# Kernel optimization log

Hardware: AMD Instinct MI355X
Metric: run time of the kernel (lower is better)

## Reference

```python
import jax, jax.numpy as jnp
import numpy as np

NQ = 16               # num_qubits
S = 1 << NQ           # 65536 superposition states
D = 128               # quantum_dim
B = 4                 # batch
ENT = 0.8             # entanglement_strength
DECO_T = 100.0        # decoherence_time


def setup_inputs() -> dict:
    key = jax.random.key(0)
    ks = jax.random.split(key, 7)
    return {
        "input_features": jax.random.normal(ks[0], (B, D), jnp.float32),
        # complex quantum_weights, stored as separate real/imag parts
        "qw_re": jax.random.normal(ks[1], (S, D), jnp.float32),
        "qw_im": jax.random.normal(ks[2], (S, D), jnp.float32),
        "rotation_angles": jax.random.normal(ks[3], (NQ, 3), jnp.float32),
        "entanglement_matrix": jax.random.normal(ks[4], (NQ, NQ), jnp.float32),
        # per-qubit measurement Linear(D, D): y = x @ W_i.T + b_i
        "meas_W": jax.random.normal(ks[5], (NQ, D, D), jnp.float32) / np.sqrt(D).astype(np.float32),
        "meas_b": jax.random.normal(ks[6], (NQ, D), jnp.float32) * np.float32(0.01),
    }


def reference(input_features, qw_re, qw_im, rotation_angles, entanglement_matrix, meas_W, meas_b):
    b = input_features.shape[0]  # input is only consulted for batch size (as in the original)
    qw = qw_re + 1j * qw_im                              # [S, D] complex64
    # ---- apply_quantum_gates: cumulative per-qubit phase = exp(i * sum of all angles)
    phase = jnp.exp(1j * rotation_angles.sum())
    state = jnp.broadcast_to((qw * phase)[None], (b, S, D))  # [B, S, D]
    # entanglement: softmax(16x16) mixes across a qubit-factored view of the state dim
    ew = jax.nn.softmax(entanglement_matrix, axis=-1).astype(state.dtype)  # [NQ, NQ]
    ent = jnp.einsum('qp,bpkd->bqkd', ew, state.reshape(b, NQ, S // NQ, D)).reshape(b, S, D)
    state = ENT * ent + (1.0 - ENT) * state
    # ---- simulate_decoherence (timer = 1 on first call)
    coh = jnp.exp(jnp.float32(-1.0 / DECO_T))
    kn = jax.random.split(jax.random.key(1), 3)
    inv_sqrt2 = np.float32(1.0 / np.sqrt(2.0))
    noise = (jax.random.normal(kn[0], (b, S, D)) + 1j * jax.random.normal(kn[1], (b, S, D))) \
            * (inv_sqrt2 * (1.0 - coh) * np.float32(0.1))
    state = state * coh + noise
    # ---- quantum_measurement: one categorical draw over S states per (batch, column)
    # multinomial(p[:, j], 1) == Gumbel-max over log p; normalization constant cancels.
    logits = jnp.log(jnp.real(state) ** 2 + jnp.imag(state) ** 2 + 1e-20)  # log |amp|^2, [B,S,D]
    u = jax.random.uniform(kn[2], (b, S, D), minval=1e-7, maxval=1.0)
    idx = jnp.argmax(logits - jnp.log(-jnp.log(u)), axis=1)  # [B, D] sampled state index
    # one-hot collapsed state; only rows 0..NQ-1 are consumed by the measurement ops,
    # so we avoid materializing the full [B, S, D] one-hot.
    measured = (idx[:, None, :] == jnp.arange(NQ)[None, :, None]).astype(jnp.float32)  # [B, NQ, D]
    outs = jnp.einsum('bnd,ned->bne', measured, meas_W) + meas_b[None]  # per-qubit Linear
    return outs.mean(axis=1)  # [B, D]
```

## Files before the change

kernel.cpp:

```cpp
#include <hip/hip_runtime.h>
#include <stdint.h>
#include <math.h>

constexpr int D_ = 128;
constexpr int KDIM = 4096;
constexpr uint32_t NTH = 4096u * 128u;

#define DELTA   0.00385f
#define RELM    1.0002f
#define WLO_PAD 1e-3f
#define EPS_CMP 1e-3f

__host__ __device__ static inline void tfround(uint32_t& x0, uint32_t& x1, int r) {
    x0 += x1;
    x1 = (x1 << r) | (x1 >> (32 - r));
    x1 ^= x0;
}

__host__ __device__ static inline void tf2x32(uint32_t k0, uint32_t k1,
                                              uint32_t x0, uint32_t x1,
                                              uint32_t& o0, uint32_t& o1) {
    uint32_t ks2 = k0 ^ k1 ^ 0x1BD11BDAu;
    x0 += k0; x1 += k1;
    tfround(x0, x1, 13); tfround(x0, x1, 15); tfround(x0, x1, 26); tfround(x0, x1, 6);
    x0 += k1;  x1 += ks2 + 1u;
    tfround(x0, x1, 17); tfround(x0, x1, 29); tfround(x0, x1, 16); tfround(x0, x1, 24);
    x0 += ks2; x1 += k0 + 2u;
    tfround(x0, x1, 13); tfround(x0, x1, 15); tfround(x0, x1, 26); tfround(x0, x1, 6);
    x0 += k0;  x1 += k1 + 3u;
    tfround(x0, x1, 17); tfround(x0, x1, 29); tfround(x0, x1, 16); tfround(x0, x1, 24);
    x0 += k1;  x1 += ks2 + 4u;
    tfround(x0, x1, 13); tfround(x0, x1, 15); tfround(x0, x1, 26); tfround(x0, x1, 6);
    x0 += ks2; x1 += k0 + 5u;
    o0 = x0; o1 = x1;
}

__device__ __forceinline__ float neglog_hybrid(float u, float nz) {
    float p4 = fmaf(nz, 0.2f, 0.25f);
    float p3 = fmaf(nz, p4, 0.33333334f);
    float p2 = fmaf(nz, p3, 0.5f);
    float poly = fmaf(nz, p2, 1.0f);
    float ts = nz * poly;
    float tl = -__logf(u);
    return (nz < 0.01f) ? ts : tl;
}

__device__ __forceinline__ float erfinv_fast(float x) {
    float w = -__logf(fmaf(-x, x, 1.0f));
    float p;
    if (w < 5.0f) {
        w -= 2.5f;
        p = 2.81022636e-08f;
        p = fmaf(p, w, 3.43273939e-07f);
        p = fmaf(p, w, -3.5233877e-06f);
        p = fmaf(p, w, -4.39150654e-06f);
        p = fmaf(p, w, 0.00021858087f);
        p = fmaf(p, w, -0.00125372503f);
        p = fmaf(p, w, -0.00417768164f);
        p = fmaf(p, w, 0.246640727f);
        p = fmaf(p, w, 1.50140941f);
    } else {
        float wt = -__logf((1.0f - x) * (1.0f + x));
        float v = sqrtf(wt) - 3.0f;
        p = -0.000200214257f;
        p = fmaf(p, v, 0.000100950558f);
        p = fmaf(p, v, 0.00134934322f);
        p = fmaf(p, v, -0.00367342844f);
        p = fmaf(p, v, 0.00573950773f);
        p = fmaf(p, v, -0.0076224613f);
        p = fmaf(p, v, 0.00943887047f);
        p = fmaf(p, v, 1.00167406f);
        p = fmaf(p, v, 2.83297682f);
    }
    return p * x;
}

__device__ __forceinline__ uint32_t ordmap(float x) {
    uint32_t u = __float_as_uint(x);
    return (u & 0x80000000u) ? ~u : (u | 0x80000000u);
}
__device__ __forceinline__ float ordunmap(uint32_t m) {
    uint32_t u = (m & 0x80000000u) ? (m & 0x7FFFFFFFu) : ~m;
    return __uint_as_float(u);
}

__global__ __launch_bounds__(512) void qsl_prep(const float* __restrict__ ang,
                                                const float* __restrict__ ent,
                                                float* __restrict__ ws_f,
                                                unsigned long long* __restrict__ keys,
                                                uint32_t* __restrict__ Mlo,
                                                float coh) {
    __shared__ float sm[16][16];
    int t = threadIdx.x;
    keys[t] = 0ULL;
    if (t < 512) Mlo[t] = 0u;
    if (t < 16) {
        float row[16];
        float m = -INFINITY;
        for (int j = 0; j < 16; j++) { row[j] = ent[t * 16 + j]; m = fmaxf(m, row[j]); }
        float s = 0.f;
        for (int j = 0; j < 16; j++) { row[j] = expf(row[j] - m); s += row[j]; }
        float inv = 1.0f / s;
        for (int j = 0; j < 16; j++) sm[t][j] = row[j] * inv;
    }
    if (t == 0) {
        float a = 0.f;
        for (int i = 0; i < 48; i++) a += ang[i];
        ws_f[256] = cosf(a);
        ws_f[257] = sinf(a);
    }
    __syncthreads();
    if (t < 256) {
        int q = t >> 4, p = t & 15;
        float c = (0.8f * coh) * sm[q][p];
        if (q == p) c += 0.2f * coh;
        ws_f[t] = c;
    }
}

__global__ __launch_bounds__(256) void qsl_bound(const float* __restrict__ qre,
                                                 const float* __restrict__ qim,
                                                 const float* __restrict__ Cg,
                                                 uint32_t* __restrict__ Mlo,
                                                 unsigned long long* __restrict__ maskArr,
                                                 float4* __restrict__ whiArr,
                                                 uint32_t kC0, uint32_t kC1) {
    const int d = threadIdx.x;
    const int y = threadIdx.y;
    const int kk = blockIdx.x * 2 + y;
    const uint32_t g = (uint32_t)kk * 128u + (uint32_t)d;

    const float pr = Cg[256], pi = Cg[257];

    float eLo[16], eHi[16];
    {
        float vr[16], vi[16];
#pragma unroll
        for (int p = 0; p < 16; p++) {
            int off = (p * KDIM + kk) * D_ + d;
            float ar = qre[off], ai = qim[off];
            vr[p] = fmaf(pr, ar, -(pi * ai));
            vi[p] = fmaf(pi, ar, pr * ai);
        }
#pragma unroll
        for (int q = 0; q < 16; q++) {
            float br = 0.f, bi = 0.f;
#pragma unroll
            for (int p = 0; p < 16; p++) {
                float c = Cg[q * 16 + p];
                br = fmaf(c, vr[p], br);
                bi = fmaf(c, vi[p], bi);
            }
            float abr = fabsf(br), abi = fabsf(bi);
            float hr = abr + DELTA, hq = abi + DELTA;
            float Phi_hi = fmaf(hr, hr, fmaf(hq, hq, 1e-20f));
            float lr = fmaxf(abr - DELTA, 0.f), lq = fmaxf(abi - DELTA, 0.f);
            float Phi_lo = fmaf(lr, lr, fmaf(lq, lq, 1e-20f));
            eLo[q] = __builtin_amdgcn_rcpf(Phi_lo);
            eHi[q] = __builtin_amdgcn_rcpf(Phi_hi);
        }
    }

    unsigned long long mask64 = 0ull;
    float whi_a[4];

#pragma unroll 1
    for (int b = 0; b < 4; b++) {
        const uint32_t nb = g + ((uint32_t)b << 23);
        float ph[16];
        float mlo_t = INFINITY, mhi_t = INFINITY;
#pragma unroll
        for (int q = 0; q < 16; q++) {
            uint32_t w0, w1;
            tf2x32(kC0, kC1, 0u, nb + ((uint32_t)q << 19), w0, w1);
            uint32_t r = w0 ^ w1;
            float f = __uint_as_float((r >> 9) | 0x3f800000u) - 1.0f;
            float nz = 1.0f - f;
            float t = neglog_hybrid(f, nz);
            float plo = t * eLo[q];
            float phi_ = t * eHi[q];
            ph[q] = phi_;
            mlo_t = fminf(mlo_t, plo);
            mhi_t = fminf(mhi_t, phi_);
        }
        uint32_t mloc = 0u;
        float thr = mlo_t * RELM;
#pragma unroll
        for (int q = 0; q < 16; q++)
            if (ph[q] <= thr) mloc |= (1u << q);
        mask64 |= ((unsigned long long)mloc) << (b * 16);

        float wlo = -__logf(mlo_t) - WLO_PAD;
        whi_a[b]  = -__logf(mhi_t);
        uint32_t mu = ordmap(wlo);
        uint32_t cur = Mlo[b * 128 + d];
        if (mu > cur) atomicMax(&Mlo[b * 128 + d], mu);
    }

    maskArr[g] = mask64;
    whiArr[g] = make_float4(whi_a[0], whi_a[1], whi_a[2], whi_a[3]);
}

__global__ __launch_bounds__(256) void qsl_resolve(const float* __restrict__ qre,
                                                   const float* __restrict__ qim,
                                                   const float* __restrict__ Cg,
                                                   const uint32_t* __restrict__ Mlo,
                                                   const unsigned long long* __restrict__ maskArr,
                                                   const float4* __restrict__ whiArr,
                                                   unsigned long long* __restrict__ keys,
                                                   uint32_t kA0, uint32_t kA1,
                                                   uint32_t kB0, uint32_t kB1,
                                                   uint32_t kC0, uint32_t kC1,
                                                   float nc) {
    const int d = threadIdx.x;
    const int y = threadIdx.y;
    const int kk = blockIdx.x * 2 + y;
    const uint32_t g = (uint32_t)kk * 128u + (uint32_t)d;

    unsigned long long mask64 = maskArr[g];
    float4 whi4 = whiArr[g];
    uint32_t m0 = Mlo[0 * 128 + d];
    uint32_t m1 = Mlo[1 * 128 + d];
    uint32_t m2 = Mlo[2 * 128 + d];
    uint32_t m3 = Mlo[3 * 128 + d];

    unsigned long long live = 0ull;
    if (!(whi4.x < ordunmap(m0) - EPS_CMP)) live |= 0xFFFFull;
    if (!(whi4.y < ordunmap(m1) - EPS_CMP)) live |= 0xFFFFull << 16;
    if (!(whi4.z < ordunmap(m2) - EPS_CMP)) live |= 0xFFFFull << 32;
    if (!(whi4.w < ordunmap(m3) - EPS_CMP)) live |= 0xFFFFull << 48;
    mask64 &= live;
    if (mask64 == 0ull) return;

    const float pr = Cg[256], pi = Cg[257];
    float vr[16], vi[16];
#pragma unroll
    for (int p = 0; p < 16; p++) {
        int off = (p * KDIM + kk) * D_ + d;
        float ar = qre[off], ai = qim[off];
        vr[p] = fmaf(pr, ar, -(pi * ai));
        vi[p] = fmaf(pi, ar, pr * ai);
    }

    const float ULO = 1e-7f;
    const float UDF = 1.0f - 1e-7f;
    const float NLO = -0.99999994f;
    const float NDF = 1.0f - NLO;

    while (mask64) {
        int bit = __ffsll(mask64) - 1;
        mask64 &= mask64 - 1ull;
        uint32_t q = (uint32_t)bit & 15u;
        int b = bit >> 4;
        uint32_t n = g + ((uint32_t)bit << 19);

        float br = 0.f, bi = 0.f;
        const float4* C4 = reinterpret_cast<const float4*>(Cg + (q << 4));
#pragma unroll
        for (int j = 0; j < 4; j++) {
            float4 c = C4[j];
            br = fmaf(c.x, vr[j*4+0], br); bi = fmaf(c.x, vi[j*4+0], bi);
            br = fmaf(c.y, vr[j*4+1], br); bi = fmaf(c.y, vi[j*4+1], bi);
            br = fmaf(c.z, vr[j*4+2], br); bi = fmaf(c.z, vi[j*4+2], bi);
            br = fmaf(c.w, vr[j*4+3], br); bi = fmaf(c.w, vi[j*4+3], bi);
        }

        uint32_t w0, w1;
        tf2x32(kC0, kC1, 0u, n, w0, w1);
        uint32_t rC = w0 ^ w1;
        tf2x32(kA0, kA1, 0u, n, w0, w1);
        uint32_t rA = w0 ^ w1;
        tf2x32(kB0, kB1, 0u, n, w0, w1);
        uint32_t rB = w0 ^ w1;

        float fu = __uint_as_float((rC >> 9) | 0x3f800000u) - 1.0f;
        float u  = __fadd_rn(__fmul_rn(fu, UDF), ULO);
        float f0 = __uint_as_float((rA >> 9) | 0x3f800000u) - 1.0f;
        float x0 = __fadd_rn(__fmul_rn(f0, NDF), NLO);
        float f1 = __uint_as_float((rB >> 9) | 0x3f800000u) - 1.0f;
        float x1 = __fadd_rn(__fmul_rn(f1, NDF), NLO);
        float nr = 1.41421356f * erfinv_fast(x0);
        float ni = 1.41421356f * erfinv_fast(x1);
        float ar = fmaf(nc, nr, br);
        float ai = fmaf(nc, ni, bi);
        float logit = __logf(fmaf(ar, ar, fmaf(ai, ai, 1e-20f)));
        float nz = 1.0f - u;
        float t = neglog_hybrid(u, nz);
        float gv = __logf(t);
        float v = logit - gv;

        uint32_t s = (q << 12) + (uint32_t)kk;
        uint32_t mu = ordmap(v);
        unsigned long long kp =
            ((unsigned long long)mu << 32) |
            (unsigned long long)(0xFFFFFFFFu - s);
        atomicMax(&keys[b * 128 + d], kp);
    }
}

__global__ __launch_bounds__(128) void qsl_out(const unsigned long long* __restrict__ keys,
                                               const float* __restrict__ mW,
                                               const float* __restrict__ mb,
                                               float* __restrict__ out) {
    int b = blockIdx.x, e = threadIdx.x;
    __shared__ uint32_t idx_s[128];
    unsigned long long kp = keys[b * 128 + e];
    idx_s[e] = 0xFFFFFFFFu - (uint32_t)(kp & 0xFFFFFFFFull);
    __syncthreads();

    float acc = 0.f;
#pragma unroll
    for (int n = 0; n < 16; n++) acc += mb[n * 128 + e];
    for (int dd = 0; dd < 128; dd++) {
        uint32_t m = idx_s[dd];
        if (m < 16u) acc += mW[(m * 128 + e) * 128 + dd];
    }
    out[b * 128 + e] = acc * 0.0625f;
}

extern "C" void kernel_launch(void* const* d_in, const int* in_sizes, int n_in,
                              void* d_out, int out_size, void* d_ws, size_t ws_size,
                              hipStream_t stream) {
    (void)in_sizes; (void)n_in; (void)out_size; (void)ws_size;
    const float* qre = (const float*)d_in[1];
    const float* qim = (const float*)d_in[2];
    const float* ang = (const float*)d_in[3];
    const float* ent = (const float*)d_in[4];
    const float* mW  = (const float*)d_in[5];
    const float* mb  = (const float*)d_in[6];
    float* out = (float*)d_out;

    char* ws = (char*)d_ws;
    float* ws_f = (float*)ws;
    unsigned long long* keys = (unsigned long long*)(ws + 4096);
    uint32_t* Mlo = (uint32_t*)(ws + 8192);
    unsigned long long* maskArr = (unsigned long long*)(ws + 12288);
    float4* whiArr = (float4*)(ws + 12288 + (size_t)NTH * 8);

    uint32_t kn[6];
    tf2x32(0u, 1u, 0u, 0u, kn[0], kn[1]);
    tf2x32(0u, 1u, 0u, 1u, kn[2], kn[3]);
    tf2x32(0u, 1u, 0u, 2u, kn[4], kn[5]);

    float coh = expf(-0.01f);
    float nc  = (0.70710678f * (1.0f - coh)) * 0.1f;

    hipLaunchKernelGGL(qsl_prep, dim3(1), dim3(512), 0, stream, ang, ent, ws_f, keys, Mlo, coh);
    hipLaunchKernelGGL(qsl_bound, dim3(2048), dim3(128, 2), 0, stream,
                       qre, qim, ws_f, Mlo, maskArr, whiArr, kn[4], kn[5]);
    hipLaunchKernelGGL(qsl_resolve, dim3(2048), dim3(128, 2), 0, stream,
                       qre, qim, ws_f, Mlo, maskArr, whiArr, keys,
                       kn[0], kn[1], kn[2], kn[3], kn[4], kn[5], nc);
    hipLaunchKernelGGL(qsl_out, dim3(4), dim3(128), 0, stream, keys, mW, mb, out);
}
```

Measured before the change: 114.8 us.

## Restructure bound kernel to loop over qubits with 4-way batched Threefry and LDS-parked bounds

```diff
diff --git a/kernel.cpp b/kernel.cpp
--- a/kernel.cpp
+++ b/kernel.cpp
@@ -7,7 +7,7 @@
 constexpr uint32_t NTH = 4096u * 128u;
 
 #define DELTA   0.00385f
-#define RELM    1.0002f
+#define RELB    1.0101f
 #define WLO_PAD 1e-3f
 #define EPS_CMP 1e-3f
 
@@ -33,6 +33,41 @@
     tfround(x0, x1, 13); tfround(x0, x1, 15); tfround(x0, x1, 26); tfround(x0, x1, 6);
     x0 += ks2; x1 += k0 + 5u;
     o0 = x0; o1 = x1;
+}
+
+__device__ __forceinline__ void tf4round(uint32_t x0[4], uint32_t x1[4], int r) {
+#pragma unroll
+    for (int i = 0; i < 4; i++) x0[i] += x1[i];
+#pragma unroll
+    for (int i = 0; i < 4; i++) x1[i] = (x1[i] << r) | (x1[i] >> (32 - r));
+#pragma unroll
+    for (int i = 0; i < 4; i++) x1[i] ^= x0[i];
+}
+
+__device__ __forceinline__ void tf2x32_x4(uint32_t k0, uint32_t k1,
+                                          uint32_t n0, uint32_t n1,
+                                          uint32_t n2, uint32_t n3,
+                                          uint32_t out[4]) {
+    uint32_t ks2 = k0 ^ k1 ^ 0x1BD11BDAu;
+    uint32_t x0[4] = {k0, k0, k0, k0};
+    uint32_t x1[4] = {n0 + k1, n1 + k1, n2 + k1, n3 + k1};
+    tf4round(x0, x1, 13); tf4round(x0, x1, 15); tf4round(x0, x1, 26); tf4round(x0, x1, 6);
+#pragma unroll
+    for (int i = 0; i < 4; i++) { x0[i] += k1;  x1[i] += ks2 + 1u; }
+    tf4round(x0, x1, 17); tf4round(x0, x1, 29); tf4round(x0, x1, 16); tf4round(x0, x1, 24);
+#pragma unroll
+    for (int i = 0; i < 4; i++) { x0[i] += ks2; x1[i] += k0 + 2u; }
+    tf4round(x0, x1, 13); tf4round(x0, x1, 15); tf4round(x0, x1, 26); tf4round(x0, x1, 6);
+#pragma unroll
+    for (int i = 0; i < 4; i++) { x0[i] += k0;  x1[i] += k1 + 3u; }
+    tf4round(x0, x1, 17); tf4round(x0, x1, 29); tf4round(x0, x1, 16); tf4round(x0, x1, 24);
+#pragma unroll
+    for (int i = 0; i < 4; i++) { x0[i] += k1;  x1[i] += ks2 + 4u; }
+    tf4round(x0, x1, 13); tf4round(x0, x1, 15); tf4round(x0, x1, 26); tf4round(x0, x1, 6);
+#pragma unroll
+    for (int i = 0; i < 4; i++) { x0[i] += ks2; x1[i] += k0 + 5u; }
+#pragma unroll
+    for (int i = 0; i < 4; i++) out[i] = x0[i] ^ x1[i];
 }
 
 __device__ __forceinline__ float neglog_hybrid(float u, float nz) {
@@ -93,7 +128,7 @@
     __shared__ float sm[16][16];
     int t = threadIdx.x;
     keys[t] = 0ULL;
-    if (t < 512) Mlo[t] = 0u;
+    Mlo[t] = 0u;
     if (t < 16) {
         float row[16];
         float m = -INFINITY;
@@ -125,80 +160,105 @@
                                                  unsigned long long* __restrict__ maskArr,
                                                  float4* __restrict__ whiArr,
                                                  uint32_t kC0, uint32_t kC1) {
+    __shared__ uint2 park[16][256];
+
     const int d = threadIdx.x;
     const int y = threadIdx.y;
+    const int tid = y * 128 + d;
     const int kk = blockIdx.x * 2 + y;
     const uint32_t g = (uint32_t)kk * 128u + (uint32_t)d;
 
     const float pr = Cg[256], pi = Cg[257];
 
-    float eLo[16], eHi[16];
-    {
-        float vr[16], vi[16];
+    float vr[16], vi[16];
+#pragma unroll
+    for (int p = 0; p < 16; p++) {
+        int off = (p * KDIM + kk) * D_ + d;
+        float ar = qre[off], ai = qim[off];
+        vr[p] = fmaf(pr, ar, -(pi * ai));
+        vi[p] = fmaf(pi, ar, pr * ai);
+    }
+
+    float mlo0 = INFINITY, mlo1 = INFINITY, mlo2 = INFINITY, mlo3 = INFINITY;
+    float mhi0 = INFINITY, mhi1 = INFINITY, mhi2 = INFINITY, mhi3 = INFINITY;
+
+#pragma unroll 1
+    for (int q = 0; q < 16; q++) {
+        float br = 0.f, bi = 0.f;
 #pragma unroll
         for (int p = 0; p < 16; p++) {
-            int off = (p * KDIM + kk) * D_ + d;
-            float ar = qre[off], ai = qim[off];
-            vr[p] = fmaf(pr, ar, -(pi * ai));
-            vi[p] = fmaf(pi, ar, pr * ai);
+            float c = Cg[q * 16 + p];
+            br = fmaf(c, vr[p], br);
+            bi = fmaf(c, vi[p], bi);
         }
-#pragma unroll
-        for (int q = 0; q < 16; q++) {
-            float br = 0.f, bi = 0.f;
-#pragma unroll
-            for (int p = 0; p < 16; p++) {
-                float c = Cg[q * 16 + p];
-                br = fmaf(c, vr[p], br);
-                bi = fmaf(c, vi[p], bi);
-            }
-            float abr = fabsf(br), abi = fabsf(bi);
-            float hr = abr + DELTA, hq = abi + DELTA;
-            float Phi_hi = fmaf(hr, hr, fmaf(hq, hq, 1e-20f));
-            float lr = fmaxf(abr - DELTA, 0.f), lq = fmaxf(abi - DELTA, 0.f);
-            float Phi_lo = fmaf(lr, lr, fmaf(lq, lq, 1e-20f));
-            eLo[q] = __builtin_amdgcn_rcpf(Phi_lo);
-            eHi[q] = __builtin_amdgcn_rcpf(Phi_hi);
-        }
-    }
-
-    unsigned long long mask64 = 0ull;
-    float whi_a[4];
-
+        float abr = fabsf(br), abi = fabsf(bi);
+        float hr = abr + DELTA, hq = abi + DELTA;
+        float Phi_hi = fmaf(hr, hr, fmaf(hq, hq, 1e-20f));
+        float lr = fmaxf(abr - DELTA, 0.f), lq = fmaxf(abi - DELTA, 0.f);
+        float Phi_lo = fmaf(lr, lr, fmaf(lq, lq, 1e-20f));
+        float eLo = __builtin_amdgcn_rcpf(Phi_lo);
+        float eHi = __builtin_amdgcn_rcpf(Phi_hi);
+
+        uint32_t n0 = g + ((uint32_t)q << 19);
+        uint32_t o[4];
+        tf2x32_x4(kC0, kC1, n0, n0 + (1u << 23), n0 + (2u << 23), n0 + (3u << 23), o);
+
+        float f0 = __uint_as_float((o[0] >> 9) | 0x3f800000u) - 1.0f;
+        float f1 = __uint_as_float((o[1] >> 9) | 0x3f800000u) - 1.0f;
+        float f2 = __uint_as_float((o[2] >> 9) | 0x3f800000u) - 1.0f;
+        float f3 = __uint_as_float((o[3] >> 9) | 0x3f800000u) - 1.0f;
+        float t0 = neglog_hybrid(f0, 1.0f - f0);
+        float t1 = neglog_hybrid(f1, 1.0f - f1);
+        float t2 = neglog_hybrid(f2, 1.0f - f2);
+        float t3 = neglog_hybrid(f3, 1.0f - f3);
+
+        float ph0 = t0 * eHi, ph1 = t1 * eHi, ph2 = t2 * eHi, ph3 = t3 * eHi;
+        mlo0 = fminf(mlo0, t0 * eLo);  mhi0 = fminf(mhi0, ph0);
+        mlo1 = fminf(mlo1, t1 * eLo);  mhi1 = fminf(mhi1, ph1);
+        mlo2 = fminf(mlo2, t2 * eLo);  mhi2 = fminf(mhi2, ph2);
+        mlo3 = fminf(mlo3, t3 * eLo);  mhi3 = fminf(mhi3, ph3);
+
+        uint32_t b01 = (__float_as_uint(ph0) >> 16) | (__float_as_uint(ph1) & 0xFFFF0000u);
+        uint32_t b23 = (__float_as_uint(ph2) >> 16) | (__float_as_uint(ph3) & 0xFFFF0000u);
+        park[q][tid] = make_uint2(b01, b23);
+    }
+
+    float wlo0 = -__logf(mlo0) - WLO_PAD;
+    float wlo1 = -__logf(mlo1) - WLO_PAD;
+    float wlo2 = -__logf(mlo2) - WLO_PAD;
+    float wlo3 = -__logf(mlo3) - WLO_PAD;
+    uint32_t mu0 = ordmap(wlo0);
+    if (mu0 > Mlo[0 * 128 + d]) atomicMax(&Mlo[0 * 128 + d], mu0);
+    uint32_t mu1 = ordmap(wlo1);
+    if (mu1 > Mlo[1 * 128 + d]) atomicMax(&Mlo[1 * 128 + d], mu1);
+    uint32_t mu2 = ordmap(wlo2);
+    if (mu2 > Mlo[2 * 128 + d]) atomicMax(&Mlo[2 * 128 + d], mu2);
+    uint32_t mu3 = ordmap(wlo3);
+    if (mu3 > Mlo[3 * 128 + d]) atomicMax(&Mlo[3 * 128 + d], mu3);
+
+    float thr0 = mlo0 * RELB, thr1 = mlo1 * RELB, thr2 = mlo2 * RELB, thr3 = mlo3 * RELB;
+    uint32_t ml0 = 0u, ml1 = 0u, ml2 = 0u, ml3 = 0u;
 #pragma unroll 1
-    for (int b = 0; b < 4; b++) {
-        const uint32_t nb = g + ((uint32_t)b << 23);
-        float ph[16];
-        float mlo_t = INFINITY, mhi_t = INFINITY;
-#pragma unroll
-        for (int q = 0; q < 16; q++) {
-            uint32_t w0, w1;
-            tf2x32(kC0, kC1, 0u, nb + ((uint32_t)q << 19), w0, w1);
-            uint32_t r = w0 ^ w1;
-            float f = __uint_as_float((r >> 9) | 0x3f800000u) - 1.0f;
-            float nz = 1.0f - f;
-            float t = neglog_hybrid(f, nz);
-            float plo = t * eLo[q];
-            float phi_ = t * eHi[q];
-            ph[q] = phi_;
-            mlo_t = fminf(mlo_t, plo);
-            mhi_t = fminf(mhi_t, phi_);
-        }
-        uint32_t mloc = 0u;
-        float thr = mlo_t * RELM;
-#pragma unroll
-        for (int q = 0; q < 16; q++)
-            if (ph[q] <= thr) mloc |= (1u << q);
-        mask64 |= ((unsigned long long)mloc) << (b * 16);
-
-        float wlo = -__logf(mlo_t) - WLO_PAD;
-        whi_a[b]  = -__logf(mhi_t);
-        uint32_t mu = ordmap(wlo);
-        uint32_t cur = Mlo[b * 128 + d];
-        if (mu > cur) atomicMax(&Mlo[b * 128 + d], mu);
-    }
+    for (int q = 0; q < 16; q++) {
+        uint2 pk = park[q][tid];
+        float p0 = __uint_as_float(pk.x << 16);
+        float p1 = __uint_as_float(pk.x & 0xFFFF0000u);
+        float p2 = __uint_as_float(pk.y << 16);
+        float p3 = __uint_as_float(pk.y & 0xFFFF0000u);
+        if (p0 <= thr0) ml0 |= (1u << q);
+        if (p1 <= thr1) ml1 |= (1u << q);
+        if (p2 <= thr2) ml2 |= (1u << q);
+        if (p3 <= thr3) ml3 |= (1u << q);
+    }
+
+    unsigned long long mask64 =
+        (unsigned long long)ml0 |
+        ((unsigned long long)ml1 << 16) |
+        ((unsigned long long)ml2 << 32) |
+        ((unsigned long long)ml3 << 48);
 
     maskArr[g] = mask64;
-    whiArr[g] = make_float4(whi_a[0], whi_a[1], whi_a[2], whi_a[3]);
+    whiArr[g] = make_float4(-__logf(mhi0), -__logf(mhi1), -__logf(mhi2), -__logf(mhi3));
 }
 
 __global__ __launch_bounds__(256) void qsl_resolve(const float* __restrict__ qre,
@@ -345,7 +405,8 @@
     float coh = expf(-0.01f);
     float nc  = (0.70710678f * (1.0f - coh)) * 0.1f;
 
-    hipLaunchKernelGGL(qsl_prep, dim3(1), dim3(512), 0, stream, ang, ent, ws_f, keys, Mlo, coh);
+    hipLaunchKernelGGL(qsl_prep, dim3(1), dim3(512), 0, stream,
+                       ang, ent, ws_f, keys, Mlo, coh);
     hipLaunchKernelGGL(qsl_bound, dim3(2048), dim3(128, 2), 0, stream,
                        qre, qim, ws_f, Mlo, maskArr, whiArr, kn[4], kn[5]);
     hipLaunchKernelGGL(qsl_resolve, dim3(2048), dim3(128, 2), 0, stream,
```

Result: slower. 135.5 us (+18.0%).
